# Performance work log

Measured on AMD Instinct MI355X. Metric: run time of the kernel, lower is better.

## Reference

```python
import jax, jax.numpy as jnp
import numpy as np

H = 128
NUM_LAYERS = 3
IN_DIM = 32


def setup_inputs() -> dict:
    key = jax.random.key(0)
    ks = jax.random.split(key, 16)
    B, L = 2, 512
    coords = jax.random.normal(ks[0], (B, L, 3), dtype=jnp.float32) * 10.0
    contacts = (jax.random.uniform(ks[1], (B, L, L)) < 0.1).astype(jnp.float32)
    node_feats = jax.random.normal(ks[2], (B, L, IN_DIM), dtype=jnp.float32)
    s = lambda fan_in: 1.0 / np.sqrt(fan_in)
    in_w = jax.random.normal(ks[3], (IN_DIM, H), dtype=jnp.float32) * s(IN_DIM)
    in_b = jnp.zeros((H,), dtype=jnp.float32)
    # per-layer stacked params
    e_w1 = jax.random.normal(ks[4], (NUM_LAYERS, 2 * H + 2, H), dtype=jnp.float32) * s(2 * H + 2)
    e_b1 = jnp.zeros((NUM_LAYERS, H), dtype=jnp.float32)
    e_w2 = jax.random.normal(ks[5], (NUM_LAYERS, H, H), dtype=jnp.float32) * s(H)
    e_b2 = jnp.zeros((NUM_LAYERS, H), dtype=jnp.float32)
    n_w1 = jax.random.normal(ks[6], (NUM_LAYERS, 2 * H, H), dtype=jnp.float32) * s(2 * H)
    n_b1 = jnp.zeros((NUM_LAYERS, H), dtype=jnp.float32)
    n_w2 = jax.random.normal(ks[7], (NUM_LAYERS, H, H), dtype=jnp.float32) * s(H)
    n_b2 = jnp.zeros((NUM_LAYERS, H), dtype=jnp.float32)
    return dict(coords=coords, contacts=contacts, node_feats=node_feats,
                in_w=in_w, in_b=in_b,
                e_w1=e_w1, e_b1=e_b1, e_w2=e_w2, e_b2=e_b2,
                n_w1=n_w1, n_b1=n_b1, n_w2=n_w2, n_b2=n_b2)


def _forward(coords, contacts, node_feats, in_w, in_b,
             e_w1, e_b1, e_w2, e_b2, n_w1, n_b1, n_w2, n_b2):
    # input projection
    h = node_feats @ in_w + in_b  # (B,L,H)
    # pairwise distances (safe norm: grad 0 on the zero diagonal)
    diff = coords[:, :, None, :] - coords[:, None, :, :]  # (B,L,L,3)
    sq = jnp.sum(diff * diff, axis=-1, keepdims=True)      # (B,L,L,1)
    dist = jnp.where(sq > 0, jnp.sqrt(jnp.where(sq > 0, sq, 1.0)), 0.0)
    contact_ij = contacts[..., None]                        # (B,L,L,1)
    edge_mask = (contacts > 0)[..., None]                   # (B,L,L,1)
    for layer in range(NUM_LAYERS):
        w1 = e_w1[layer]
        # split the first edge-linear over the concat [hi, hj, dist, contact]
        hi_part = h @ w1[:H]              # (B,L,H) -> broadcast over j
        hj_part = h @ w1[H:2 * H]         # (B,L,H) -> broadcast over i
        pre = (hi_part[:, :, None, :] + hj_part[:, None, :, :]
               + dist * w1[2 * H] + contact_ij * w1[2 * H + 1] + e_b1[layer])
        m_ij = jax.nn.silu(jax.nn.silu(pre) @ e_w2[layer] + e_b2[layer])  # (B,L,L,H)
        m_i = jnp.sum(jnp.where(edge_mask, m_ij, 0.0), axis=2)            # (B,L,H)
        # node MLP on concat([h, m_i]) via split linear
        w1n = n_w1[layer]
        npre = h @ w1n[:H] + m_i @ w1n[H:] + n_b1[layer]
        delta_h = jax.nn.silu(npre) @ n_w2[layer] + n_b2[layer]
        h = h + delta_h
    return h


def reference(coords, contacts, node_feats, in_w, in_b,
              e_w1, e_b1, e_w2, e_b2, n_w1, n_b1, n_w2, n_b2):
    return _forward(coords, contacts, node_feats, in_w, in_b,
                    e_w1, e_b1, e_w2, e_b2, n_w1, n_b1, n_w2, n_b2)
```

## Files before the change

kernel.cpp:

```cpp
#include <hip/hip_runtime.h>
#include <hip/hip_bf16.h>


#define Hc 128
#define Lc 512
#define ROWS 1024

typedef __bf16 bf16x8 __attribute__((ext_vector_type(8)));
typedef float  f32x4  __attribute__((ext_vector_type(4)));

__device__ __forceinline__ float silu(float x) {
    return x / (1.f + __expf(-x));
}

__global__ __launch_bounds__(64) void build_edges(
    const float* __restrict__ contacts,
    unsigned short* __restrict__ elist, int* __restrict__ ecnt) {
    int r = blockIdx.x;
    int lane = threadIdx.x;
    const float* row = contacts + (size_t)r * Lc;
    int cnt = 0;
    for (int base = 0; base < Lc; base += 64) {
        float v = row[base + lane];
        unsigned long long mask = __ballot(v > 0.f);
        if (v > 0.f) {
            int pos = cnt + __popcll(mask & ((1ull << lane) - 1ull));
            elist[r * Lc + pos] = (unsigned short)(base + lane);
        }
        cnt += __popcll(mask);
    }
    if (lane == 0) ecnt[r] = cnt;
}

__global__ __launch_bounds__(256) void prep_wbf(
    const float* __restrict__ in_w, const float* __restrict__ e_w1,
    const float* __restrict__ e_w2, const float* __restrict__ n_w1,
    const float* __restrict__ n_w2,
    __bf16* __restrict__ in_wt, __bf16* __restrict__ w1et,
    __bf16* __restrict__ w2te, __bf16* __restrict__ w1nt,
    __bf16* __restrict__ w2nt) {
    int idx = blockIdx.x * 256 + threadIdx.x;
    if (idx < 4096) {
        int col = idx >> 5, k = idx & 31;
        in_wt[idx] = (__bf16)in_w[k * Hc + col];
    } else if (idx < 4096 + 98304) {
        int q = idx - 4096;
        int l = q / 32768, r = q % 32768;
        int col = r >> 7, k = r & 127;
        float v = (col < 128) ? e_w1[(size_t)l * 258 * Hc + k * Hc + col]
                              : e_w1[(size_t)l * 258 * Hc + (128 + k) * Hc + (col - 128)];
        w1et[q] = (__bf16)v;
    } else if (idx < 4096 + 98304 + 49152) {
        int q = idx - 4096 - 98304;
        int l = q / 16384, r = q % 16384;
        int col = r >> 7, k = r & 127;
        w2te[q] = (__bf16)e_w2[(size_t)l * 16384 + k * Hc + col];
    } else if (idx < 4096 + 98304 + 49152 + 98304) {
        int q = idx - 4096 - 98304 - 49152;
        int l = q / 32768, r = q % 32768;
        int col = r >> 8, k = r & 255;
        w1nt[q] = (__bf16)n_w1[(size_t)l * 32768 + k * Hc + col];
    } else {
        int q = idx - 4096 - 98304 - 49152 - 98304;
        int l = q / 16384, r = q % 16384;
        int col = r >> 7, k = r & 127;
        w2nt[q] = (__bf16)n_w2[(size_t)l * 16384 + k * Hc + col];
    }
}

__global__ __launch_bounds__(256) void input_mfma(
    const float* __restrict__ nf, const __bf16* __restrict__ in_wt,
    const float* __restrict__ in_b,
    const __bf16* __restrict__ w1et0, const float* __restrict__ b1e,
    const float* __restrict__ fold,
    float* __restrict__ h, float* __restrict__ hi, float* __restrict__ hj) {
    int r0 = blockIdx.x * 16;
    int t = threadIdx.x;
    int l = t & 63, w = t >> 6;
    int lr = l & 15, g = l >> 4;
    __shared__ __bf16 A0[16 * 32];
    __shared__ __bf16 A3[16 * Hc];

    if (t < 64) {
        int row = t >> 2, blk = t & 3, k0 = blk * 8;
        const float* src = &nf[(size_t)(r0 + row) * 32 + k0];
        float4 v0 = *(const float4*)src, v1 = *(const float4*)(src + 4);
        bf16x8 o;
        o[0] = (__bf16)v0.x; o[1] = (__bf16)v0.y; o[2] = (__bf16)v0.z; o[3] = (__bf16)v0.w;
        o[4] = (__bf16)v1.x; o[5] = (__bf16)v1.y; o[6] = (__bf16)v1.z; o[7] = (__bf16)v1.w;
        *(bf16x8*)&A0[row * 32 + (blk ^ (row & 3)) * 8] = o;
    }
    int c0 = w * 32;
    bf16x8 bf0[2];
#pragma unroll
    for (int nt = 0; nt < 2; nt++)
        bf0[nt] = *(const bf16x8*)&in_wt[(size_t)(c0 + nt * 16 + lr) * 32 + g * 8];
    __syncthreads();
    f32x4 acc[2] = {};
    {
        bf16x8 a = *(const bf16x8*)&A0[lr * 32 + (g ^ (lr & 3)) * 8];
        acc[0] = __builtin_amdgcn_mfma_f32_16x16x32_bf16(a, bf0[0], acc[0], 0, 0, 0);
        acc[1] = __builtin_amdgcn_mfma_f32_16x16x32_bf16(a, bf0[1], acc[1], 0, 0, 0);
    }
#pragma unroll
    for (int nt = 0; nt < 2; nt++) {
        int col = c0 + nt * 16 + lr;
        float bb = in_b[col];
#pragma unroll
        for (int j = 0; j < 4; j++) {
            int row = g * 4 + j;
            float hv = acc[nt][j] + bb;
            h[(size_t)(r0 + row) * Hc + col] = hv;
            A3[row * Hc + ((col >> 3) ^ (row & 7)) * 8 + (col & 7)] = (__bf16)hv;
        }
    }
    __syncthreads();
    int c3 = w * 64;
    bf16x8 b3[4][4];
#pragma unroll
    for (int nt = 0; nt < 4; nt++)
#pragma unroll
        for (int ks = 0; ks < 4; ks++)
            b3[nt][ks] = *(const bf16x8*)&w1et0[
                (size_t)(c3 + nt * 16 + lr) * Hc + ks * 32 + g * 8];
    f32x4 acc3[4] = {};
#pragma unroll
    for (int ks = 0; ks < 4; ks++) {
        bf16x8 a = *(const bf16x8*)&A3[lr * Hc + (((ks * 4 + g) ^ (lr & 7))) * 8];
#pragma unroll
        for (int nt = 0; nt < 4; nt++)
            acc3[nt] = __builtin_amdgcn_mfma_f32_16x16x32_bf16(a, b3[nt][ks], acc3[nt], 0, 0, 0);
    }
#pragma unroll
    for (int nt = 0; nt < 4; nt++) {
        int col = c3 + nt * 16 + lr;
#pragma unroll
        for (int j = 0; j < 4; j++) {
            int row = g * 4 + j;
            if (col < 128)
                hi[(size_t)(r0 + row) * Hc + col] = acc3[nt][j] + b1e[col] + fold[col];
            else
                hj[(size_t)(r0 + row) * Hc + (col - 128)] = acc3[nt][j];
        }
    }
}

__global__ __launch_bounds__(256) void edge_kernel(
    const float* __restrict__ hi, const float* __restrict__ hj,
    const float* __restrict__ coords,
    const unsigned short* __restrict__ elist, const int* __restrict__ ecnt,
    const float* __restrict__ w1d, const __bf16* __restrict__ w2t,
    const float* __restrict__ b2, float* __restrict__ m_out) {
    int r = blockIdx.x;
    int b = r >> 9;
    int i = r & (Lc - 1);
    int t = threadIdx.x;
    int l = t & 63, w = t >> 6;

    __shared__ __bf16 S[32 * Hc];
    __shared__ float dL[Lc];
    __shared__ unsigned short jLs[Lc];

    int cnt = ecnt[r];

    float cx = coords[(b * Lc + i) * 3 + 0];
    float cy = coords[(b * Lc + i) * 3 + 1];
    float cz = coords[(b * Lc + i) * 3 + 2];
    for (int e = t; e < cnt; e += 256) {
        int j = elist[r * Lc + e];
        float dx = cx - coords[(b * Lc + j) * 3 + 0];
        float dy = cy - coords[(b * Lc + j) * 3 + 1];
        float dz = cz - coords[(b * Lc + j) * 3 + 2];
        dL[e] = sqrtf(dx * dx + dy * dy + dz * dz);
        jLs[e] = (unsigned short)j;
    }

    int e_f = t >> 3;
    int cg  = t & 7;
    int c0  = cg * 16;
    float4 hi4[4], wd4[4];
#pragma unroll
    for (int q = 0; q < 4; q++) {
        hi4[q] = *(const float4*)&hi[(size_t)r * Hc + c0 + q * 4];
        wd4[q] = *(const float4*)&w1d[c0 + q * 4];
    }

    bf16x8 bf[2][4];
#pragma unroll
    for (int nt = 0; nt < 2; nt++)
#pragma unroll
        for (int kk = 0; kk < 4; kk++)
            bf[nt][kk] = *(const bf16x8*)&w2t[
                (size_t)(w * 32 + nt * 16 + (l & 15)) * Hc + kk * 32 + (l >> 4) * 8];

    float b2v[2] = { b2[w * 32 + (l & 15)], b2[w * 32 + 16 + (l & 15)] };
    float msum[2] = { 0.f, 0.f };

    __syncthreads();

    int row0 = l & 15, g = l >> 4, swz = l & 7;
    for (int base = 0; base < cnt; base += 32) {
        bf16x8 o0, o1;
        if (base + e_f < cnt) {
            int j = jLs[base + e_f];
            float d = dL[base + e_f];
            const float* hjrow = hj + ((size_t)(b * Lc + j)) * Hc + c0;
            float v[16];
#pragma unroll
            for (int q = 0; q < 4; q++) {
                float4 hjv = *(const float4*)&hjrow[q * 4];
                v[q * 4 + 0] = silu(hi4[q].x + hjv.x + d * wd4[q].x);
                v[q * 4 + 1] = silu(hi4[q].y + hjv.y + d * wd4[q].y);
                v[q * 4 + 2] = silu(hi4[q].z + hjv.z + d * wd4[q].z);
                v[q * 4 + 3] = silu(hi4[q].w + hjv.w + d * wd4[q].w);
            }
#pragma unroll
            for (int u = 0; u < 8; u++) {
                o0[u] = (__bf16)v[u];
                o1[u] = (__bf16)v[8 + u];
            }
        } else {
#pragma unroll
            for (int u = 0; u < 8; u++) { o0[u] = (__bf16)0.f; o1[u] = (__bf16)0.f; }
        }
        int sw = e_f & 7;
        *(bf16x8*)&S[e_f * Hc + ((cg * 2) ^ sw) * 8]     = o0;
        *(bf16x8*)&S[e_f * Hc + ((cg * 2 + 1) ^ sw) * 8] = o1;
        __syncthreads();

        f32x4 acc[2][2] = {};
#pragma unroll
        for (int kk = 0; kk < 4; kk++) {
            bf16x8 a0 = *(const bf16x8*)&S[row0 * Hc + (((kk * 4 + g) ^ swz)) * 8];
            bf16x8 a1 = *(const bf16x8*)&S[(16 + row0) * Hc + (((kk * 4 + g) ^ swz)) * 8];
            acc[0][0] = __builtin_amdgcn_mfma_f32_16x16x32_bf16(a0, bf[0][kk], acc[0][0], 0, 0, 0);
            acc[0][1] = __builtin_amdgcn_mfma_f32_16x16x32_bf16(a0, bf[1][kk], acc[0][1], 0, 0, 0);
            acc[1][0] = __builtin_amdgcn_mfma_f32_16x16x32_bf16(a1, bf[0][kk], acc[1][0], 0, 0, 0);
            acc[1][1] = __builtin_amdgcn_mfma_f32_16x16x32_bf16(a1, bf[1][kk], acc[1][1], 0, 0, 0);
        }

#pragma unroll
        for (int mt = 0; mt < 2; mt++)
#pragma unroll
            for (int nt = 0; nt < 2; nt++)
#pragma unroll
                for (int jj = 0; jj < 4; jj++) {
                    int er = mt * 16 + g * 4 + jj;
                    if (base + er < cnt)
                        msum[nt] += silu(acc[mt][nt][jj] + b2v[nt]);
                }
        __syncthreads();
    }

    float v0 = msum[0]; v0 += __shfl_xor(v0, 16); v0 += __shfl_xor(v0, 32);
    float v1 = msum[1]; v1 += __shfl_xor(v1, 16); v1 += __shfl_xor(v1, 32);
    if (l < 16) {
        m_out[(size_t)r * Hc + w * 32 + l]      = v0;
        m_out[(size_t)r * Hc + w * 32 + 16 + l] = v1;
    }
}

__global__ __launch_bounds__(256) void node_mfma(
    const float* __restrict__ h, const float* __restrict__ m,
    const __bf16* __restrict__ w1nt, const float* __restrict__ b1n,
    const __bf16* __restrict__ w2nt, const float* __restrict__ b2n,
    float* __restrict__ hout, int do_hij,
    const __bf16* __restrict__ w1et, const float* __restrict__ b1e,
    const float* __restrict__ fold,
    float* __restrict__ hi, float* __restrict__ hj) {
    int r0 = blockIdx.x * 16;
    int t = threadIdx.x;
    int l = t & 63, w = t >> 6;
    int lr = l & 15, g = l >> 4;
    __shared__ __bf16 A1[16 * 256];
    __shared__ __bf16 A2[16 * Hc];
    __shared__ __bf16 A3[16 * Hc];
    __shared__ float hbuf[16 * Hc];

#pragma unroll
    for (int it = 0; it < 2; it++) {
        int idx = t + it * 256;
        int row = idx >> 5, blk = idx & 31, k0 = blk * 8;
        const float* src = (k0 < 128)
            ? &h[(size_t)(r0 + row) * Hc + k0]
            : &m[(size_t)(r0 + row) * Hc + (k0 - 128)];
        float4 v0 = *(const float4*)src, v1 = *(const float4*)(src + 4);
        bf16x8 o;
        o[0] = (__bf16)v0.x; o[1] = (__bf16)v0.y; o[2] = (__bf16)v0.z; o[3] = (__bf16)v0.w;
        o[4] = (__bf16)v1.x; o[5] = (__bf16)v1.y; o[6] = (__bf16)v1.z; o[7] = (__bf16)v1.w;
        *(bf16x8*)&A1[row * 256 + (blk ^ (row & 7)) * 8] = o;
        if (k0 < 128) {
            *(float4*)&hbuf[row * Hc + k0] = v0;
            *(float4*)&hbuf[row * Hc + k0 + 4] = v1;
        }
    }
    int c0 = w * 32;
    bf16x8 b1f[2][8];
#pragma unroll
    for (int nt = 0; nt < 2; nt++)
#pragma unroll
        for (int ks = 0; ks < 8; ks++)
            b1f[nt][ks] = *(const bf16x8*)&w1nt[
                (size_t)(c0 + nt * 16 + lr) * 256 + ks * 32 + g * 8];
    __syncthreads();

    f32x4 acc[2] = {};
#pragma unroll
    for (int ks = 0; ks < 8; ks++) {
        bf16x8 a = *(const bf16x8*)&A1[lr * 256 + (((ks * 4 + g) ^ (lr & 7))) * 8];
        acc[0] = __builtin_amdgcn_mfma_f32_16x16x32_bf16(a, b1f[0][ks], acc[0], 0, 0, 0);
        acc[1] = __builtin_amdgcn_mfma_f32_16x16x32_bf16(a, b1f[1][ks], acc[1], 0, 0, 0);
    }
#pragma unroll
    for (int nt = 0; nt < 2; nt++) {
        int col = c0 + nt * 16 + lr;
        float bb = b1n[col];
#pragma unroll
        for (int j = 0; j < 4; j++) {
            int row = g * 4 + j;
            A2[row * Hc + ((col >> 3) ^ (row & 7)) * 8 + (col & 7)] =
                (__bf16)silu(acc[nt][j] + bb);
        }
    }
    __syncthreads();

    bf16x8 b2f[2][4];
#pragma unroll
    for (int nt = 0; nt < 2; nt++)
#pragma unroll
        for (int ks = 0; ks < 4; ks++)
            b2f[nt][ks] = *(const bf16x8*)&w2nt[
                (size_t)(c0 + nt * 16 + lr) * Hc + ks * 32 + g * 8];
    f32x4 acc2[2] = {};
#pragma unroll
    for (int ks = 0; ks < 4; ks++) {
        bf16x8 a = *(const bf16x8*)&A2[lr * Hc + (((ks * 4 + g) ^ (lr & 7))) * 8];
        acc2[0] = __builtin_amdgcn_mfma_f32_16x16x32_bf16(a, b2f[0][ks], acc2[0], 0, 0, 0);
        acc2[1] = __builtin_amdgcn_mfma_f32_16x16x32_bf16(a, b2f[1][ks], acc2[1], 0, 0, 0);
    }
#pragma unroll
    for (int nt = 0; nt < 2; nt++) {
        int col = c0 + nt * 16 + lr;
        float bb = b2n[col];
#pragma unroll
        for (int j = 0; j < 4; j++) {
            int row = g * 4 + j;
            float hnew = hbuf[row * Hc + col] + acc2[nt][j] + bb;
            hout[(size_t)(r0 + row) * Hc + col] = hnew;
            A3[row * Hc + ((col >> 3) ^ (row & 7)) * 8 + (col & 7)] = (__bf16)hnew;
        }
    }
    if (!do_hij) return;
    __syncthreads();

    int c3 = w * 64;
    bf16x8 b3[4][4];
#pragma unroll
    for (int nt = 0; nt < 4; nt++)
#pragma unroll
        for (int ks = 0; ks < 4; ks++)
            b3[nt][ks] = *(const bf16x8*)&w1et[
                (size_t)(c3 + nt * 16 + lr) * Hc + ks * 32 + g * 8];
    f32x4 acc3[4] = {};
#pragma unroll
    for (int ks = 0; ks < 4; ks++) {
        bf16x8 a = *(const bf16x8*)&A3[lr * Hc + (((ks * 4 + g) ^ (lr & 7))) * 8];
#pragma unroll
        for (int nt = 0; nt < 4; nt++)
            acc3[nt] = __builtin_amdgcn_mfma_f32_16x16x32_bf16(a, b3[nt][ks], acc3[nt], 0, 0, 0);
    }
#pragma unroll
    for (int nt = 0; nt < 4; nt++) {
        int col = c3 + nt * 16 + lr;
#pragma unroll
        for (int j = 0; j < 4; j++) {
            int row = g * 4 + j;
            if (col < 128)
                hi[(size_t)(r0 + row) * Hc + col] = acc3[nt][j] + b1e[col] + fold[col];
            else
                hj[(size_t)(r0 + row) * Hc + (col - 128)] = acc3[nt][j];
        }
    }
}

extern "C" void kernel_launch(void* const* d_in, const int* in_sizes, int n_in,
                              void* d_out, int out_size, void* d_ws, size_t ws_size,
                              hipStream_t stream) {
    const float* coords     = (const float*)d_in[0];
    const float* contacts   = (const float*)d_in[1];
    const float* node_feats = (const float*)d_in[2];
    const float* in_w       = (const float*)d_in[3];
    const float* in_b       = (const float*)d_in[4];
    const float* e_w1       = (const float*)d_in[5];
    const float* e_b1       = (const float*)d_in[6];
    const float* e_w2       = (const float*)d_in[7];
    const float* e_b2       = (const float*)d_in[8];
    const float* n_w1       = (const float*)d_in[9];
    const float* n_b1       = (const float*)d_in[10];
    const float* n_w2       = (const float*)d_in[11];
    const float* n_b2       = (const float*)d_in[12];

    float* ws = (float*)d_ws;
    float* h  = ws;
    float* hi = ws + 131072;
    float* hj = ws + 262144;
    float* m  = ws + 393216;
    unsigned short* elist = (unsigned short*)(ws + 524288);
    int*   ecnt = (int*)(ws + 786432);
    __bf16* in_wt = (__bf16*)(ws + 787456);
    __bf16* w1et  = (__bf16*)(ws + 789504);
    __bf16* w2te  = (__bf16*)(ws + 838656);
    __bf16* w1nt  = (__bf16*)(ws + 863232);
    __bf16* w2nt  = (__bf16*)(ws + 912384);

    prep_wbf<<<1168, 256, 0, stream>>>(in_w, e_w1, e_w2, n_w1, n_w2,
                                       in_wt, w1et, w2te, w1nt, w2nt);
    build_edges<<<ROWS, 64, 0, stream>>>(contacts, elist, ecnt);
    input_mfma<<<ROWS / 16, 256, 0, stream>>>(
        node_feats, in_wt, in_b,
        w1et, e_b1, e_w1 + (size_t)257 * Hc,
        h, hi, hj);

    for (int l = 0; l < 3; l++) {
        const float* w1 = e_w1 + (size_t)l * 258 * Hc;
        edge_kernel<<<ROWS, 256, 0, stream>>>(hi, hj, coords, elist, ecnt,
                                              w1 + 2 * Hc * Hc,
                                              w2te + (size_t)l * Hc * Hc,
                                              e_b2 + l * Hc, m);
        int do_hij = (l < 2);
        int lnext = (l + 1 < 3) ? l + 1 : 0;
        float* hout = (l == 2) ? (float*)d_out : h;
        node_mfma<<<ROWS / 16, 256, 0, stream>>>(
            h, m,
            w1nt + (size_t)l * 128 * 256, n_b1 + l * Hc,
            w2nt + (size_t)l * 128 * 128, n_b2 + l * Hc,
            hout, do_hij,
            w1et + (size_t)lnext * 256 * 128, e_b1 + lnext * Hc,
            e_w1 + (size_t)lnext * 258 * Hc + (size_t)257 * Hc,
            hi, hj);
    }
}
```

Measured before the change: 167.9 us.

## Merge edge-list and weight prep kernels; widen edge tile to 64 with inline distances

Fuses build_edges into the weight-conversion kernel so one launch handles both. The edge kernel now processes 64 edges per iteration instead of 32, with each thread handling 32 channels. It computes distances and neighbor indices inline rather than staging them in shared memory first, and drops one barrier per iteration. The aim is fewer launches, fewer loop iterations and barriers, and more MFMA work per shared-memory tile. In exchange it uses more accumulator registers and more shared memory, and reloads hi and w1d from memory on every edge.

```diff
diff --git a/kernel.cpp b/kernel.cpp
--- a/kernel.cpp
+++ b/kernel.cpp
@@ -13,33 +13,34 @@
     return x / (1.f + __expf(-x));
 }
 
-__global__ __launch_bounds__(64) void build_edges(
+__global__ __launch_bounds__(256) void prep_all(
     const float* __restrict__ contacts,
-    unsigned short* __restrict__ elist, int* __restrict__ ecnt) {
-    int r = blockIdx.x;
-    int lane = threadIdx.x;
-    const float* row = contacts + (size_t)r * Lc;
-    int cnt = 0;
-    for (int base = 0; base < Lc; base += 64) {
-        float v = row[base + lane];
-        unsigned long long mask = __ballot(v > 0.f);
-        if (v > 0.f) {
-            int pos = cnt + __popcll(mask & ((1ull << lane) - 1ull));
-            elist[r * Lc + pos] = (unsigned short)(base + lane);
-        }
-        cnt += __popcll(mask);
-    }
-    if (lane == 0) ecnt[r] = cnt;
-}
-
-__global__ __launch_bounds__(256) void prep_wbf(
+    unsigned short* __restrict__ elist, int* __restrict__ ecnt,
     const float* __restrict__ in_w, const float* __restrict__ e_w1,
     const float* __restrict__ e_w2, const float* __restrict__ n_w1,
     const float* __restrict__ n_w2,
     __bf16* __restrict__ in_wt, __bf16* __restrict__ w1et,
     __bf16* __restrict__ w2te, __bf16* __restrict__ w1nt,
     __bf16* __restrict__ w2nt) {
-    int idx = blockIdx.x * 256 + threadIdx.x;
+    int blk = blockIdx.x;
+    if (blk < 256) {
+        int r = blk * 4 + (threadIdx.x >> 6);
+        int lane = threadIdx.x & 63;
+        const float* row = contacts + (size_t)r * Lc;
+        int cnt = 0;
+        for (int base = 0; base < Lc; base += 64) {
+            float v = row[base + lane];
+            unsigned long long mask = __ballot(v > 0.f);
+            if (v > 0.f) {
+                int pos = cnt + __popcll(mask & ((1ull << lane) - 1ull));
+                elist[r * Lc + pos] = (unsigned short)(base + lane);
+            }
+            cnt += __popcll(mask);
+        }
+        if (lane == 0) ecnt[r] = cnt;
+        return;
+    }
+    int idx = (blk - 256) * 256 + threadIdx.x;
     if (idx < 4096) {
         int col = idx >> 5, k = idx & 31;
         in_wt[idx] = (__bf16)in_w[k * Hc + col];
@@ -156,100 +157,91 @@
     int i = r & (Lc - 1);
     int t = threadIdx.x;
     int l = t & 63, w = t >> 6;
-
-    __shared__ __bf16 S[32 * Hc];
-    __shared__ float dL[Lc];
-    __shared__ unsigned short jLs[Lc];
+    int lr = l & 15, g = l >> 4;
+
+    __shared__ __bf16 S[64 * Hc];
 
     int cnt = ecnt[r];
 
+    bf16x8 bf[2][4];
+#pragma unroll
+    for (int nt = 0; nt < 2; nt++)
+#pragma unroll
+        for (int kk = 0; kk < 4; kk++)
+            bf[nt][kk] = *(const bf16x8*)&w2t[
+                (size_t)(w * 32 + nt * 16 + lr) * Hc + kk * 32 + g * 8];
+    float b2v[2] = { b2[w * 32 + lr], b2[w * 32 + 16 + lr] };
+    float msum[2] = { 0.f, 0.f };
+
+    int e_f = t >> 2;
+    int cq  = t & 3;
+    int c0  = cq * 32;
     float cx = coords[(b * Lc + i) * 3 + 0];
     float cy = coords[(b * Lc + i) * 3 + 1];
     float cz = coords[(b * Lc + i) * 3 + 2];
-    for (int e = t; e < cnt; e += 256) {
-        int j = elist[r * Lc + e];
-        float dx = cx - coords[(b * Lc + j) * 3 + 0];
-        float dy = cy - coords[(b * Lc + j) * 3 + 1];
-        float dz = cz - coords[(b * Lc + j) * 3 + 2];
-        dL[e] = sqrtf(dx * dx + dy * dy + dz * dz);
-        jLs[e] = (unsigned short)j;
-    }
-
-    int e_f = t >> 3;
-    int cg  = t & 7;
-    int c0  = cg * 16;
-    float4 hi4[4], wd4[4];
-#pragma unroll
-    for (int q = 0; q < 4; q++) {
-        hi4[q] = *(const float4*)&hi[(size_t)r * Hc + c0 + q * 4];
-        wd4[q] = *(const float4*)&w1d[c0 + q * 4];
-    }
-
-    bf16x8 bf[2][4];
-#pragma unroll
-    for (int nt = 0; nt < 2; nt++)
-#pragma unroll
-        for (int kk = 0; kk < 4; kk++)
-            bf[nt][kk] = *(const bf16x8*)&w2t[
-                (size_t)(w * 32 + nt * 16 + (l & 15)) * Hc + kk * 32 + (l >> 4) * 8];
-
-    float b2v[2] = { b2[w * 32 + (l & 15)], b2[w * 32 + 16 + (l & 15)] };
-    float msum[2] = { 0.f, 0.f };
-
-    __syncthreads();
-
-    int row0 = l & 15, g = l >> 4, swz = l & 7;
-    for (int base = 0; base < cnt; base += 32) {
-        bf16x8 o0, o1;
+    const float* hjb   = hj + (size_t)(b * Lc) * Hc;
+    const float* hirow = hi + (size_t)r * Hc + c0;
+    const float* wdrow = w1d + c0;
+
+    for (int base = 0; base < cnt; base += 64) {
+        if (base) __syncthreads();
         if (base + e_f < cnt) {
-            int j = jLs[base + e_f];
-            float d = dL[base + e_f];
-            const float* hjrow = hj + ((size_t)(b * Lc + j)) * Hc + c0;
-            float v[16];
-#pragma unroll
-            for (int q = 0; q < 4; q++) {
-                float4 hjv = *(const float4*)&hjrow[q * 4];
-                v[q * 4 + 0] = silu(hi4[q].x + hjv.x + d * wd4[q].x);
-                v[q * 4 + 1] = silu(hi4[q].y + hjv.y + d * wd4[q].y);
-                v[q * 4 + 2] = silu(hi4[q].z + hjv.z + d * wd4[q].z);
-                v[q * 4 + 3] = silu(hi4[q].w + hjv.w + d * wd4[q].w);
-            }
-#pragma unroll
-            for (int u = 0; u < 8; u++) {
-                o0[u] = (__bf16)v[u];
-                o1[u] = (__bf16)v[8 + u];
+            int j = elist[r * Lc + base + e_f];
+            float dx = cx - coords[(b * Lc + j) * 3 + 0];
+            float dy = cy - coords[(b * Lc + j) * 3 + 1];
+            float dz = cz - coords[(b * Lc + j) * 3 + 2];
+            float d = sqrtf(dx * dx + dy * dy + dz * dz);
+            const float* hjrow = hjb + (size_t)j * Hc + c0;
+#pragma unroll
+            for (int p = 0; p < 4; p++) {
+                float4 ha = *(const float4*)&hjrow[p * 8];
+                float4 hb = *(const float4*)&hjrow[p * 8 + 4];
+                float4 ia = *(const float4*)&hirow[p * 8];
+                float4 ib = *(const float4*)&hirow[p * 8 + 4];
+                float4 wa = *(const float4*)&wdrow[p * 8];
+                float4 wb = *(const float4*)&wdrow[p * 8 + 4];
+                bf16x8 o;
+                o[0] = (__bf16)silu(ia.x + ha.x + d * wa.x);
+                o[1] = (__bf16)silu(ia.y + ha.y + d * wa.y);
+                o[2] = (__bf16)silu(ia.z + ha.z + d * wa.z);
+                o[3] = (__bf16)silu(ia.w + ha.w + d * wa.w);
+                o[4] = (__bf16)silu(ib.x + hb.x + d * wb.x);
+                o[5] = (__bf16)silu(ib.y + hb.y + d * wb.y);
+                o[6] = (__bf16)silu(ib.z + hb.z + d * wb.z);
+                o[7] = (__bf16)silu(ib.w + hb.w + d * wb.w);
+                *(bf16x8*)&S[e_f * Hc + ((cq * 4 + p) ^ (e_f & 7)) * 8] = o;
             }
         } else {
-#pragma unroll
-            for (int u = 0; u < 8; u++) { o0[u] = (__bf16)0.f; o1[u] = (__bf16)0.f; }
-        }
-        int sw = e_f & 7;
-        *(bf16x8*)&S[e_f * Hc + ((cg * 2) ^ sw) * 8]     = o0;
-        *(bf16x8*)&S[e_f * Hc + ((cg * 2 + 1) ^ sw) * 8] = o1;
+            bf16x8 z = {};
+#pragma unroll
+            for (int p = 0; p < 4; p++)
+                *(bf16x8*)&S[e_f * Hc + ((cq * 4 + p) ^ (e_f & 7)) * 8] = z;
+        }
         __syncthreads();
 
-        f32x4 acc[2][2] = {};
-#pragma unroll
-        for (int kk = 0; kk < 4; kk++) {
-            bf16x8 a0 = *(const bf16x8*)&S[row0 * Hc + (((kk * 4 + g) ^ swz)) * 8];
-            bf16x8 a1 = *(const bf16x8*)&S[(16 + row0) * Hc + (((kk * 4 + g) ^ swz)) * 8];
-            acc[0][0] = __builtin_amdgcn_mfma_f32_16x16x32_bf16(a0, bf[0][kk], acc[0][0], 0, 0, 0);
-            acc[0][1] = __builtin_amdgcn_mfma_f32_16x16x32_bf16(a0, bf[1][kk], acc[0][1], 0, 0, 0);
-            acc[1][0] = __builtin_amdgcn_mfma_f32_16x16x32_bf16(a1, bf[0][kk], acc[1][0], 0, 0, 0);
-            acc[1][1] = __builtin_amdgcn_mfma_f32_16x16x32_bf16(a1, bf[1][kk], acc[1][1], 0, 0, 0);
-        }
-
-#pragma unroll
-        for (int mt = 0; mt < 2; mt++)
+        f32x4 acc[4][2] = {};
+#pragma unroll
+        for (int ks = 0; ks < 4; ks++) {
+            bf16x8 a[4];
+#pragma unroll
+            for (int mt = 0; mt < 4; mt++)
+                a[mt] = *(const bf16x8*)&S[(mt * 16 + lr) * Hc + ((ks * 4 + g) ^ (lr & 7)) * 8];
+#pragma unroll
+            for (int mt = 0; mt < 4; mt++) {
+                acc[mt][0] = __builtin_amdgcn_mfma_f32_16x16x32_bf16(a[mt], bf[0][ks], acc[mt][0], 0, 0, 0);
+                acc[mt][1] = __builtin_amdgcn_mfma_f32_16x16x32_bf16(a[mt], bf[1][ks], acc[mt][1], 0, 0, 0);
+            }
+        }
+
+#pragma unroll
+        for (int mt = 0; mt < 4; mt++)
 #pragma unroll
             for (int nt = 0; nt < 2; nt++)
 #pragma unroll
                 for (int jj = 0; jj < 4; jj++) {
-                    int er = mt * 16 + g * 4 + jj;
-                    if (base + er < cnt)
+                    if (base + mt * 16 + g * 4 + jj < cnt)
                         msum[nt] += silu(acc[mt][nt][jj] + b2v[nt]);
                 }
-        __syncthreads();
     }
 
     float v0 = msum[0]; v0 += __shfl_xor(v0, 16); v0 += __shfl_xor(v0, 32);
@@ -413,9 +405,10 @@
     __bf16* w1nt  = (__bf16*)(ws + 863232);
     __bf16* w2nt  = (__bf16*)(ws + 912384);
 
-    prep_wbf<<<1168, 256, 0, stream>>>(in_w, e_w1, e_w2, n_w1, n_w2,
-                                       in_wt, w1et, w2te, w1nt, w2nt);
-    build_edges<<<ROWS, 64, 0, stream>>>(contacts, elist, ecnt);
+    prep_all<<<256 + 1168, 256, 0, stream>>>(
+        contacts, elist, ecnt,
+        in_w, e_w1, e_w2, n_w1, n_w2,
+        in_wt, w1et, w2te, w1nt, w2nt);
     input_mfma<<<ROWS / 16, 256, 0, stream>>>(
         node_feats, in_wt, in_b,
         w1et, e_b1, e_w1 + (size_t)257 * Hc,
```

New measurement: 193.1 us. 1.15x slower.

## Split edge rows across two blocks, merge prep kernels, sum partials in node kernel

Applied to the files above, without the earlier changes.

The edge kernel now launches two blocks per node row, and each takes alternating 32-edge chunks. Each block writes a partial message sum, and the node kernel adds the two partials while loading. The per-row shared-memory precompute of distances and neighbour indices is dropped, so distances are computed inline per chunk, and the trailing barrier is removed. The edge-list build is folded into the weight-conversion kernel to save a launch. The aim is more parallelism and occupancy in the dominant edge stage, at the cost of an extra partial buffer and duplicated weight-fragment loads per block.

```diff
diff --git a/kernel.cpp b/kernel.cpp
--- a/kernel.cpp
+++ b/kernel.cpp
@@ -13,33 +13,34 @@
     return x / (1.f + __expf(-x));
 }
 
-__global__ __launch_bounds__(64) void build_edges(
+__global__ __launch_bounds__(256) void prep_all(
     const float* __restrict__ contacts,
-    unsigned short* __restrict__ elist, int* __restrict__ ecnt) {
-    int r = blockIdx.x;
-    int lane = threadIdx.x;
-    const float* row = contacts + (size_t)r * Lc;
-    int cnt = 0;
-    for (int base = 0; base < Lc; base += 64) {
-        float v = row[base + lane];
-        unsigned long long mask = __ballot(v > 0.f);
-        if (v > 0.f) {
-            int pos = cnt + __popcll(mask & ((1ull << lane) - 1ull));
-            elist[r * Lc + pos] = (unsigned short)(base + lane);
-        }
-        cnt += __popcll(mask);
-    }
-    if (lane == 0) ecnt[r] = cnt;
-}
-
-__global__ __launch_bounds__(256) void prep_wbf(
+    unsigned short* __restrict__ elist, int* __restrict__ ecnt,
     const float* __restrict__ in_w, const float* __restrict__ e_w1,
     const float* __restrict__ e_w2, const float* __restrict__ n_w1,
     const float* __restrict__ n_w2,
     __bf16* __restrict__ in_wt, __bf16* __restrict__ w1et,
     __bf16* __restrict__ w2te, __bf16* __restrict__ w1nt,
     __bf16* __restrict__ w2nt) {
-    int idx = blockIdx.x * 256 + threadIdx.x;
+    int blk = blockIdx.x;
+    if (blk < 256) {
+        int r = blk * 4 + (threadIdx.x >> 6);
+        int lane = threadIdx.x & 63;
+        const float* row = contacts + (size_t)r * Lc;
+        int cnt = 0;
+        for (int base = 0; base < Lc; base += 64) {
+            float v = row[base + lane];
+            unsigned long long mask = __ballot(v > 0.f);
+            if (v > 0.f) {
+                int pos = cnt + __popcll(mask & ((1ull << lane) - 1ull));
+                elist[r * Lc + pos] = (unsigned short)(base + lane);
+            }
+            cnt += __popcll(mask);
+        }
+        if (lane == 0) ecnt[r] = cnt;
+        return;
+    }
+    int idx = (blk - 256) * 256 + threadIdx.x;
     if (idx < 4096) {
         int col = idx >> 5, k = idx & 31;
         in_wt[idx] = (__bf16)in_w[k * Hc + col];
@@ -150,61 +151,55 @@
     const float* __restrict__ coords,
     const unsigned short* __restrict__ elist, const int* __restrict__ ecnt,
     const float* __restrict__ w1d, const __bf16* __restrict__ w2t,
-    const float* __restrict__ b2, float* __restrict__ m_out) {
-    int r = blockIdx.x;
+    const float* __restrict__ b2, float* __restrict__ m_part) {
+    int r = blockIdx.x >> 1, half = blockIdx.x & 1;
     int b = r >> 9;
     int i = r & (Lc - 1);
     int t = threadIdx.x;
     int l = t & 63, w = t >> 6;
+    int lr = l & 15, g = l >> 4;
 
     __shared__ __bf16 S[32 * Hc];
-    __shared__ float dL[Lc];
-    __shared__ unsigned short jLs[Lc];
-
+
+    float* mp = m_part + ((size_t)half * ROWS + r) * Hc;
     int cnt = ecnt[r];
 
-    float cx = coords[(b * Lc + i) * 3 + 0];
-    float cy = coords[(b * Lc + i) * 3 + 1];
-    float cz = coords[(b * Lc + i) * 3 + 2];
-    for (int e = t; e < cnt; e += 256) {
-        int j = elist[r * Lc + e];
-        float dx = cx - coords[(b * Lc + j) * 3 + 0];
-        float dy = cy - coords[(b * Lc + j) * 3 + 1];
-        float dz = cz - coords[(b * Lc + j) * 3 + 2];
-        dL[e] = sqrtf(dx * dx + dy * dy + dz * dz);
-        jLs[e] = (unsigned short)j;
-    }
+    bf16x8 bf[2][4];
+#pragma unroll
+    for (int nt = 0; nt < 2; nt++)
+#pragma unroll
+        for (int kk = 0; kk < 4; kk++)
+            bf[nt][kk] = *(const bf16x8*)&w2t[
+                (size_t)(w * 32 + nt * 16 + lr) * Hc + kk * 32 + g * 8];
+    float b2v[2] = { b2[w * 32 + lr], b2[w * 32 + 16 + lr] };
+    float msum[2] = { 0.f, 0.f };
 
     int e_f = t >> 3;
     int cg  = t & 7;
     int c0  = cg * 16;
+    float cxi = coords[(b * Lc + i) * 3 + 0];
+    float cyi = coords[(b * Lc + i) * 3 + 1];
+    float czi = coords[(b * Lc + i) * 3 + 2];
     float4 hi4[4], wd4[4];
 #pragma unroll
     for (int q = 0; q < 4; q++) {
         hi4[q] = *(const float4*)&hi[(size_t)r * Hc + c0 + q * 4];
         wd4[q] = *(const float4*)&w1d[c0 + q * 4];
     }
-
-    bf16x8 bf[2][4];
-#pragma unroll
-    for (int nt = 0; nt < 2; nt++)
-#pragma unroll
-        for (int kk = 0; kk < 4; kk++)
-            bf[nt][kk] = *(const bf16x8*)&w2t[
-                (size_t)(w * 32 + nt * 16 + (l & 15)) * Hc + kk * 32 + (l >> 4) * 8];
-
-    float b2v[2] = { b2[w * 32 + (l & 15)], b2[w * 32 + 16 + (l & 15)] };
-    float msum[2] = { 0.f, 0.f };
-
-    __syncthreads();
-
-    int row0 = l & 15, g = l >> 4, swz = l & 7;
-    for (int base = 0; base < cnt; base += 32) {
+    const float* hjb = hj + (size_t)(b * Lc) * Hc;
+
+    int first = half * 32;
+    for (int base = first; base < cnt; base += 64) {
+        if (base != first) __syncthreads();
+        int nloc = cnt - base; if (nloc > 32) nloc = 32;
         bf16x8 o0, o1;
-        if (base + e_f < cnt) {
-            int j = jLs[base + e_f];
-            float d = dL[base + e_f];
-            const float* hjrow = hj + ((size_t)(b * Lc + j)) * Hc + c0;
+        if (e_f < nloc) {
+            int j = elist[r * Lc + base + e_f];
+            float dx = cxi - coords[(b * Lc + j) * 3 + 0];
+            float dy = cyi - coords[(b * Lc + j) * 3 + 1];
+            float dz = czi - coords[(b * Lc + j) * 3 + 2];
+            float d = sqrtf(dx * dx + dy * dy + dz * dz);
+            const float* hjrow = hjb + (size_t)j * Hc + c0;
             float v[16];
 #pragma unroll
             for (int q = 0; q < 4; q++) {
@@ -230,13 +225,13 @@
 
         f32x4 acc[2][2] = {};
 #pragma unroll
-        for (int kk = 0; kk < 4; kk++) {
-            bf16x8 a0 = *(const bf16x8*)&S[row0 * Hc + (((kk * 4 + g) ^ swz)) * 8];
-            bf16x8 a1 = *(const bf16x8*)&S[(16 + row0) * Hc + (((kk * 4 + g) ^ swz)) * 8];
-            acc[0][0] = __builtin_amdgcn_mfma_f32_16x16x32_bf16(a0, bf[0][kk], acc[0][0], 0, 0, 0);
-            acc[0][1] = __builtin_amdgcn_mfma_f32_16x16x32_bf16(a0, bf[1][kk], acc[0][1], 0, 0, 0);
-            acc[1][0] = __builtin_amdgcn_mfma_f32_16x16x32_bf16(a1, bf[0][kk], acc[1][0], 0, 0, 0);
-            acc[1][1] = __builtin_amdgcn_mfma_f32_16x16x32_bf16(a1, bf[1][kk], acc[1][1], 0, 0, 0);
+        for (int ks = 0; ks < 4; ks++) {
+            bf16x8 a0 = *(const bf16x8*)&S[lr * Hc + ((ks * 4 + g) ^ (lr & 7)) * 8];
+            bf16x8 a1 = *(const bf16x8*)&S[(16 + lr) * Hc + ((ks * 4 + g) ^ (lr & 7)) * 8];
+            acc[0][0] = __builtin_amdgcn_mfma_f32_16x16x32_bf16(a0, bf[0][ks], acc[0][0], 0, 0, 0);
+            acc[0][1] = __builtin_amdgcn_mfma_f32_16x16x32_bf16(a0, bf[1][ks], acc[0][1], 0, 0, 0);
+            acc[1][0] = __builtin_amdgcn_mfma_f32_16x16x32_bf16(a1, bf[0][ks], acc[1][0], 0, 0, 0);
+            acc[1][1] = __builtin_amdgcn_mfma_f32_16x16x32_bf16(a1, bf[1][ks], acc[1][1], 0, 0, 0);
         }
 
 #pragma unroll
@@ -245,23 +240,22 @@
             for (int nt = 0; nt < 2; nt++)
 #pragma unroll
                 for (int jj = 0; jj < 4; jj++) {
-                    int er = mt * 16 + g * 4 + jj;
-                    if (base + er < cnt)
+                    if (mt * 16 + g * 4 + jj < nloc)
                         msum[nt] += silu(acc[mt][nt][jj] + b2v[nt]);
                 }
-        __syncthreads();
     }
 
     float v0 = msum[0]; v0 += __shfl_xor(v0, 16); v0 += __shfl_xor(v0, 32);
     float v1 = msum[1]; v1 += __shfl_xor(v1, 16); v1 += __shfl_xor(v1, 32);
     if (l < 16) {
-        m_out[(size_t)r * Hc + w * 32 + l]      = v0;
-        m_out[(size_t)r * Hc + w * 32 + 16 + l] = v1;
+        mp[w * 32 + l]      = v0;
+        mp[w * 32 + 16 + l] = v1;
     }
 }
 
 __global__ __launch_bounds__(256) void node_mfma(
-    const float* __restrict__ h, const float* __restrict__ m,
+    const float* __restrict__ h, const float* __restrict__ m0,
+    const float* __restrict__ m1,
     const __bf16* __restrict__ w1nt, const float* __restrict__ b1n,
     const __bf16* __restrict__ w2nt, const float* __restrict__ b2n,
     float* __restrict__ hout, int do_hij,
@@ -281,18 +275,26 @@
     for (int it = 0; it < 2; it++) {
         int idx = t + it * 256;
         int row = idx >> 5, blk = idx & 31, k0 = blk * 8;
-        const float* src = (k0 < 128)
-            ? &h[(size_t)(r0 + row) * Hc + k0]
-            : &m[(size_t)(r0 + row) * Hc + (k0 - 128)];
-        float4 v0 = *(const float4*)src, v1 = *(const float4*)(src + 4);
+        float4 v0, v1;
+        if (k0 < 128) {
+            const float* src = &h[(size_t)(r0 + row) * Hc + k0];
+            v0 = *(const float4*)src; v1 = *(const float4*)(src + 4);
+            *(float4*)&hbuf[row * Hc + k0] = v0;
+            *(float4*)&hbuf[row * Hc + k0 + 4] = v1;
+        } else {
+            const float* s0 = &m0[(size_t)(r0 + row) * Hc + (k0 - 128)];
+            const float* s1 = &m1[(size_t)(r0 + row) * Hc + (k0 - 128)];
+            float4 a0 = *(const float4*)s0, a1 = *(const float4*)(s0 + 4);
+            float4 c0v = *(const float4*)s1, c1 = *(const float4*)(s1 + 4);
+            v0.x = a0.x + c0v.x; v0.y = a0.y + c0v.y;
+            v0.z = a0.z + c0v.z; v0.w = a0.w + c0v.w;
+            v1.x = a1.x + c1.x; v1.y = a1.y + c1.y;
+            v1.z = a1.z + c1.z; v1.w = a1.w + c1.w;
+        }
         bf16x8 o;
         o[0] = (__bf16)v0.x; o[1] = (__bf16)v0.y; o[2] = (__bf16)v0.z; o[3] = (__bf16)v0.w;
         o[4] = (__bf16)v1.x; o[5] = (__bf16)v1.y; o[6] = (__bf16)v1.z; o[7] = (__bf16)v1.w;
         *(bf16x8*)&A1[row * 256 + (blk ^ (row & 7)) * 8] = o;
-        if (k0 < 128) {
-            *(float4*)&hbuf[row * Hc + k0] = v0;
-            *(float4*)&hbuf[row * Hc + k0 + 4] = v1;
-        }
     }
     int c0 = w * 32;
     bf16x8 b1f[2][8];
@@ -404,7 +406,6 @@
     float* h  = ws;
     float* hi = ws + 131072;
     float* hj = ws + 262144;
-    float* m  = ws + 393216;
     unsigned short* elist = (unsigned short*)(ws + 524288);
     int*   ecnt = (int*)(ws + 786432);
     __bf16* in_wt = (__bf16*)(ws + 787456);
@@ -412,10 +413,14 @@
     __bf16* w2te  = (__bf16*)(ws + 838656);
     __bf16* w1nt  = (__bf16*)(ws + 863232);
     __bf16* w2nt  = (__bf16*)(ws + 912384);
-
-    prep_wbf<<<1168, 256, 0, stream>>>(in_w, e_w1, e_w2, n_w1, n_w2,
-                                       in_wt, w1et, w2te, w1nt, w2nt);
-    build_edges<<<ROWS, 64, 0, stream>>>(contacts, elist, ecnt);
+    float* m_part = ws + 936960;
+    float* m0 = m_part;
+    float* m1 = m_part + 131072;
+
+    prep_all<<<256 + 1168, 256, 0, stream>>>(
+        contacts, elist, ecnt,
+        in_w, e_w1, e_w2, n_w1, n_w2,
+        in_wt, w1et, w2te, w1nt, w2nt);
     input_mfma<<<ROWS / 16, 256, 0, stream>>>(
         node_feats, in_wt, in_b,
         w1et, e_b1, e_w1 + (size_t)257 * Hc,
@@ -423,15 +428,15 @@
 
     for (int l = 0; l < 3; l++) {
         const float* w1 = e_w1 + (size_t)l * 258 * Hc;
-        edge_kernel<<<ROWS, 256, 0, stream>>>(hi, hj, coords, elist, ecnt,
-                                              w1 + 2 * Hc * Hc,
-                                              w2te + (size_t)l * Hc * Hc,
-                                              e_b2 + l * Hc, m);
+        edge_kernel<<<ROWS * 2, 256, 0, stream>>>(hi, hj, coords, elist, ecnt,
+                                                  w1 + 2 * Hc * Hc,
+                                                  w2te + (size_t)l * Hc * Hc,
+                                                  e_b2 + l * Hc, m_part);
         int do_hij = (l < 2);
         int lnext = (l + 1 < 3) ? l + 1 : 0;
         float* hout = (l == 2) ? (float*)d_out : h;
         node_mfma<<<ROWS / 16, 256, 0, stream>>>(
-            h, m,
+            h, m0, m1,
             w1nt + (size_t)l * 128 * 256, n_b1 + l * Hc,
             w2nt + (size_t)l * 128 * 128, n_b2 + l * Hc,
             hout, do_hij,
```

Result: slower. 184.6 us (+9.9%).
